# Kernel optimization log

Measured on AMD Instinct MI355X. Metric: run time of the kernel, lower is better.

Reference implementation:

```python
import jax, jax.numpy as jnp
import numpy as np

B, T, C, H, N = 4, 1024, 2048, 32, 64
DFF, DW, DV, DA, DG = 8192, 64, 32, 64, 128
GN_EPS = 64e-5  # RWKV7 ln_x GroupNorm eps


def _ln(x, w, b, eps=1e-5):
    m = x.mean(-1, keepdims=True)
    v = ((x - m) ** 2).mean(-1, keepdims=True)
    return (x - m) / jnp.sqrt(v + eps) * w + b


def _block(x, v_first, att_shift, ffn_shift, wkv_state,
           ln1_w, ln1_b, ln2_w, ln2_b,
           x_r, x_w, x_k, x_v, x_a, x_g,
           Wr, Wk, Wv, Wo,
           w0, w1, w2, v0, v1, v2, a0, a1, a2, g1, g2,
           k_k, k_a, r_k, lnx_w, lnx_b,
           ffn_xk, Wk_ffn, Wv_ffn):
    # ----- TimeMix -----
    xn = _ln(x, ln1_w, ln1_b)
    xx = jnp.concatenate([att_shift[:, None, :], xn[:, :-1]], axis=1) - xn
    xr = xn + xx * x_r
    xw = xn + xx * x_w
    xk_ = xn + xx * x_k
    xv = xn + xx * x_v
    xa = xn + xx * x_a
    xg = xn + xx * x_g

    r = xr @ Wr
    w = -jax.nn.softplus(-(w0 + jnp.tanh(xw @ w1) @ w2)) - 0.5  # <= -0.5
    k = xk_ @ Wk
    v = xv @ Wv
    # layer_id != 0: interpolate toward v_first
    v = v + (v_first - v) * jax.nn.sigmoid(v0 + (xv @ v1) @ v2)
    a = jax.nn.sigmoid(a0 + (xa @ a1) @ a2)
    g = jax.nn.sigmoid(xg @ g1) @ g2

    kk = (k * k_k).reshape(B, T, H, N)
    kk = kk / jnp.maximum(jnp.linalg.norm(kk, axis=-1, keepdims=True), 1e-12)
    k = k * (1.0 + (a - 1.0) * k_a)

    rh = r.reshape(B, T, H, N)
    wh = jnp.exp(-jnp.exp(w.reshape(B, T, H, N)))  # decay in (0,1)
    kh = k.reshape(B, T, H, N)
    vh = v.reshape(B, T, H, N)
    ah = a.reshape(B, T, H, N)
    aa = -kk
    bb = kk * ah

    def step(S, inp):
        # S: [B,H,N(value),N(key)]
        r_t, w_t, k_t, v_t, a_t, b_t = inp
        sa = jnp.einsum('bhvk,bhk->bhv', S, a_t)
        S = S * w_t[:, :, None, :] + sa[..., None] * b_t[:, :, None, :] + v_t[..., None] * k_t[:, :, None, :]
        y = jnp.einsum('bhvk,bhk->bhv', S, r_t)
        return S, y

    tm = lambda z: jnp.swapaxes(z, 0, 1)  # [B,T,H,N] -> [T,B,H,N]
    S_new, ys = jax.lax.scan(step, wkv_state, (tm(rh), tm(wh), tm(kh), tm(vh), tm(aa), tm(bb)))
    x_wkv = jnp.swapaxes(ys, 0, 1).reshape(B, T, C)

    # GroupNorm over H groups of size N (RWKV7 ln_x)
    xh = x_wkv.reshape(B, T, H, N)
    mu = xh.mean(-1, keepdims=True)
    var = ((xh - mu) ** 2).mean(-1, keepdims=True)
    x_wkv = ((xh - mu) / jnp.sqrt(var + GN_EPS)).reshape(B, T, C) * lnx_w + lnx_b

    resid = ((rh * kh * r_k).sum(-1, keepdims=True) * vh).reshape(B, T, C)
    x_wkv = x_wkv + resid
    att_out = (x_wkv * g) @ Wo
    x1 = x + att_out

    # ----- ChannelMix -----
    xn2 = _ln(x1, ln2_w, ln2_b)
    xx2 = jnp.concatenate([ffn_shift[:, None, :], xn2[:, :-1]], axis=1) - xn2
    xkf = xn2 + xx2 * ffn_xk
    kf = jnp.square(jax.nn.relu(xkf @ Wk_ffn))
    x_out = x1 + kf @ Wv_ffn
    return x_out, S_new


def setup_inputs() -> dict:
    ks = jax.random.split(jax.random.key(0), 48)
    rn = lambda i, sh, s=1.0: jax.random.normal(ks[i], sh, dtype=jnp.float32) * s
    return {
        'x': rn(0, (B, T, C)), 'v_first': rn(1, (B, T, C)),
        'att_shift': rn(2, (B, C)), 'ffn_shift': rn(3, (B, C)),
        'wkv_state': jnp.zeros((B, H, N, N), jnp.float32),
        'ln1_w': jnp.ones((C,), jnp.float32), 'ln1_b': jnp.zeros((C,), jnp.float32),
        'ln2_w': jnp.ones((C,), jnp.float32), 'ln2_b': jnp.zeros((C,), jnp.float32),
        'x_r': rn(4, (C,), 0.3), 'x_w': rn(5, (C,), 0.3), 'x_k': rn(6, (C,), 0.3),
        'x_v': rn(7, (C,), 0.3), 'x_a': rn(8, (C,), 0.3), 'x_g': rn(9, (C,), 0.3),
        'Wr': rn(10, (C, C), 0.02), 'Wk': rn(11, (C, C), 0.02),
        'Wv': rn(12, (C, C), 0.02), 'Wo': rn(13, (C, C), 0.02),
        'w0': rn(14, (C,), 0.3), 'w1': rn(15, (C, DW), 0.02), 'w2': rn(16, (DW, C), 0.02),
        'v0': rn(17, (C,), 0.3), 'v1': rn(18, (C, DV), 0.02), 'v2': rn(19, (DV, C), 0.02),
        'a0': rn(20, (C,), 0.3), 'a1': rn(21, (C, DA), 0.02), 'a2': rn(22, (DA, C), 0.02),
        'g1': rn(23, (C, DG), 0.02), 'g2': rn(24, (DG, C), 0.02),
        'k_k': rn(25, (C,), 0.1) + 0.7, 'k_a': rn(26, (C,), 0.1) + 0.7, 'r_k': rn(27, (H, N), 0.1),
        'lnx_w': jnp.ones((C,), jnp.float32), 'lnx_b': jnp.zeros((C,), jnp.float32),
        'ffn_xk': rn(28, (C,), 0.3), 'Wk_ffn': rn(29, (C, DFF), 0.02), 'Wv_ffn': rn(30, (DFF, C), 0.02),
    }


def reference(x, v_first, att_shift, ffn_shift, wkv_state,
              ln1_w, ln1_b, ln2_w, ln2_b,
              x_r, x_w, x_k, x_v, x_a, x_g,
              Wr, Wk, Wv, Wo,
              w0, w1, w2, v0, v1, v2, a0, a1, a2, g1, g2,
              k_k, k_a, r_k, lnx_w, lnx_b,
              ffn_xk, Wk_ffn, Wv_ffn):
    return _block(x, v_first, att_shift, ffn_shift, wkv_state,
                  ln1_w, ln1_b, ln2_w, ln2_b,
                  x_r, x_w, x_k, x_v, x_a, x_g,
                  Wr, Wk, Wv, Wo,
                  w0, w1, w2, v0, v1, v2, a0, a1, a2, g1, g2,
                  k_k, k_a, r_k, lnx_w, lnx_b,
                  ffn_xk, Wk_ffn, Wv_ffn)
```

## Files before the change

### kernel.cpp

```cpp
#include <hip/hip_runtime.h>
#include <cstdint>


typedef __attribute__((ext_vector_type(4))) float f32x4;
typedef __attribute__((ext_vector_type(8))) __bf16 bf16x8;
typedef __attribute__((ext_vector_type(8))) unsigned short us8;

#define DEV __device__ __forceinline__

DEV unsigned short f2b(float f) {
  union { float f; unsigned u; } v; v.f = f;
  unsigned r = v.u + 0x7fffu + ((v.u >> 16) & 1u);
  return (unsigned short)(r >> 16);
}
DEV float b2f(unsigned short u) {
  union { unsigned u; float f; } v; v.u = (unsigned)u << 16;
  return v.f;
}

DEV void gload16(const void* g, void* l) {
  void* gg = const_cast<void*>(g);
  __builtin_amdgcn_global_load_lds(
      (__attribute__((address_space(1))) unsigned int*)gg,
      (__attribute__((address_space(3))) unsigned int*)l, 16, 0, 0);
}

DEV float red8(float v) {
  v += __shfl_xor(v, 1);
  v += __shfl_xor(v, 2);
  v += __shfl_xor(v, 4);
  return v;
}


__global__ void k_transpose(const float* __restrict__ src,
                            unsigned short* __restrict__ dst, int R, int Cc) {
  __shared__ float tile[32][33];
  const int c0 = blockIdx.x * 32, r0 = blockIdx.y * 32;
  const int tx = threadIdx.x, ty = threadIdx.y;
  for (int i = ty; i < 32; i += 8)
    tile[i][tx] = src[(size_t)(r0 + i) * Cc + c0 + tx];
  __syncthreads();
  for (int i = ty; i < 32; i += 8)
    dst[(size_t)(c0 + i) * R + r0 + tx] = f2b(tile[tx][i]);
}

__global__ void k_wcat(const float* __restrict__ w1, const float* __restrict__ a1,
                       const float* __restrict__ v1, const float* __restrict__ g1,
                       const float* __restrict__ xw, const float* __restrict__ xa,
                       const float* __restrict__ xv, const float* __restrict__ xg,
                       unsigned short* __restrict__ dst) {
  const int i = blockIdx.x * 256 + threadIdx.x;
  if (i >= 384 * 4096) return;
  const int j = i >> 12, c = i & 4095;
  float val = 0.f;
  if (j < 288) {
    const float* W; const float* mix; int jj, D;
    if (j < 64)       { W = w1; mix = xw; jj = j;       D = 64;  }
    else if (j < 128) { W = a1; mix = xa; jj = j - 64;  D = 64;  }
    else if (j < 160) { W = v1; mix = xv; jj = j - 128; D = 32;  }
    else              { W = g1; mix = xg; jj = j - 160; D = 128; }
    const int cc = c & 2047;
    val = W[(size_t)cc * D + jj];
    if (c >= 2048) val *= mix[cc];
  }
  dst[i] = f2b(val);
}


DEV void breduce2(float& a, float& b, float* rbuf) {
#pragma unroll
  for (int m = 1; m < 64; m <<= 1) { a += __shfl_xor(a, m); b += __shfl_xor(b, m); }
  const int wid = threadIdx.x >> 6, lane = threadIdx.x & 63;
  if (lane == 0) { rbuf[wid] = a; rbuf[4 + wid] = b; }
  __syncthreads();
  a = rbuf[0] + rbuf[1] + rbuf[2] + rbuf[3];
  b = rbuf[4] + rbuf[5] + rbuf[6] + rbuf[7];
  __syncthreads();
}

__global__ __launch_bounds__(256)
void k_ln1_mix(const float* __restrict__ x, const float* __restrict__ shift,
               const float* __restrict__ lw, const float* __restrict__ lb,
               const float* __restrict__ mr, const float* __restrict__ mk,
               const float* __restrict__ mv,
               unsigned short* __restrict__ A2, unsigned short* __restrict__ xrb,
               unsigned short* __restrict__ xkb, unsigned short* __restrict__ xvb) {
  __shared__ float rbuf[8];
  const int m = blockIdx.x, tid = threadIdx.x;
  const int b = m >> 10, t = m & 1023;
  const float* xt = x + (size_t)m * 2048 + tid * 8;
  const float* xp = (t > 0) ? (x + (size_t)(m - 1) * 2048 + tid * 8)
                            : (shift + (size_t)b * 2048 + tid * 8);
  float vt[8], vp[8];
  *(float4*)&vt[0] = *(const float4*)(xt);
  *(float4*)&vt[4] = *(const float4*)(xt + 4);
  *(float4*)&vp[0] = *(const float4*)(xp);
  *(float4*)&vp[4] = *(const float4*)(xp + 4);
  float st = 0.f, sp = 0.f;
#pragma unroll
  for (int i = 0; i < 8; ++i) { st += vt[i]; sp += vp[i]; }
  breduce2(st, sp, rbuf);
  const float mt_ = st * (1.f / 2048.f), mp_ = sp * (1.f / 2048.f);
  float qt = 0.f, qp = 0.f;
#pragma unroll
  for (int i = 0; i < 8; ++i) {
    float d0 = vt[i] - mt_; qt += d0 * d0;
    float d1 = vp[i] - mp_; qp += d1 * d1;
  }
  breduce2(qt, qp, rbuf);
  const float rt = rsqrtf(qt * (1.f / 2048.f) + 1e-5f);
  const float rp = rsqrtf(qp * (1.f / 2048.f) + 1e-5f);
  const bool lnp = (t > 0);
#pragma unroll
  for (int i = 0; i < 8; ++i) {
    const int c = tid * 8 + i;
    const float wv = lw[c], bv = lb[c];
    const float xn = (vt[i] - mt_) * rt * wv + bv;
    const float pn = lnp ? ((vp[i] - mp_) * rp * wv + bv) : vp[i];
    const float xx = pn - xn;
    A2[(size_t)m * 4096 + c] = f2b(xn);
    A2[(size_t)m * 4096 + 2048 + c] = f2b(xx);
    xrb[(size_t)m * 2048 + c] = f2b(xn + xx * mr[c]);
    xkb[(size_t)m * 2048 + c] = f2b(xn + xx * mk[c]);
    xvb[(size_t)m * 2048 + c] = f2b(xn + xx * mv[c]);
  }
}

__global__ __launch_bounds__(256)
void k_ln2_mix(const float* __restrict__ x1, const float* __restrict__ shift,
               const float* __restrict__ lw, const float* __restrict__ lb,
               const float* __restrict__ mk, unsigned short* __restrict__ xkf) {
  __shared__ float rbuf[8];
  const int m = blockIdx.x, tid = threadIdx.x;
  const int b = m >> 10, t = m & 1023;
  const float* xt = x1 + (size_t)m * 2048 + tid * 8;
  const float* xp = (t > 0) ? (x1 + (size_t)(m - 1) * 2048 + tid * 8)
                            : (shift + (size_t)b * 2048 + tid * 8);
  float vt[8], vp[8];
  *(float4*)&vt[0] = *(const float4*)(xt);
  *(float4*)&vt[4] = *(const float4*)(xt + 4);
  *(float4*)&vp[0] = *(const float4*)(xp);
  *(float4*)&vp[4] = *(const float4*)(xp + 4);
  float st = 0.f, sp = 0.f;
#pragma unroll
  for (int i = 0; i < 8; ++i) { st += vt[i]; sp += vp[i]; }
  breduce2(st, sp, rbuf);
  const float mt_ = st * (1.f / 2048.f), mp_ = sp * (1.f / 2048.f);
  float qt = 0.f, qp = 0.f;
#pragma unroll
  for (int i = 0; i < 8; ++i) {
    float d0 = vt[i] - mt_; qt += d0 * d0;
    float d1 = vp[i] - mp_; qp += d1 * d1;
  }
  breduce2(qt, qp, rbuf);
  const float rt = rsqrtf(qt * (1.f / 2048.f) + 1e-5f);
  const float rp = rsqrtf(qp * (1.f / 2048.f) + 1e-5f);
  const bool lnp = (t > 0);
#pragma unroll
  for (int i = 0; i < 8; ++i) {
    const int c = tid * 8 + i;
    const float wv = lw[c], bv = lb[c];
    const float xn = (vt[i] - mt_) * rt * wv + bv;
    const float pn = lnp ? ((vp[i] - mp_) * rp * wv + bv) : vp[i];
    xkf[(size_t)m * 2048 + c] = f2b(xn + (pn - xn) * mk[c]);
  }
}


constexpr int EP_F32 = 0, EP_B16 = 1, EP_W = 2, EP_AB16 = 3, EP_VGB16 = 4,
              EP_RELU2 = 5, EP_ADDF = 6, EP_HACT = 7;

template <int EP>
DEV void ep_store(float acc, long row, long c, long ldc, float* Co,
                  unsigned short* Cob, const float* bias, const float* e0f,
                  const unsigned short* e0b) {
  const long idx = row * ldc + c;
  if constexpr (EP == EP_F32) {
    Co[idx] = acc;
  } else if constexpr (EP == EP_B16) {
    Cob[idx] = f2b(acc);
  } else if constexpr (EP == EP_W) {
    const float wv = bias[c] + acc;
    const float sp = log1pf(expf(-wv));
    const float w = -sp - 0.5f;
    Co[idx] = expf(-expf(w));
  } else if constexpr (EP == EP_AB16) {
    Cob[idx] = f2b(1.f / (1.f + expf(-(bias[c] + acc))));
  } else if constexpr (EP == EP_VGB16) {
    const float s = 1.f / (1.f + expf(-(bias[c] + acc)));
    const float vv = b2f(e0b[idx]);
    Cob[idx] = f2b(vv + (e0f[idx] - vv) * s);
  } else if constexpr (EP == EP_RELU2) {
    const float r = fmaxf(acc, 0.f);
    Cob[idx] = f2b(r * r);
  } else if constexpr (EP == EP_ADDF) {
    Co[idx] = acc + e0f[idx];
  } else if constexpr (EP == EP_HACT) {
    float vv = acc;
    if (c < 64) vv = tanhf(vv);
    else if (c >= 160) vv = 1.f / (1.f + expf(-vv));
    Cob[idx] = f2b(vv);
  }
}

template <int EP>
__global__ __launch_bounds__(256)
void gemm_bt(const unsigned short* __restrict__ A, long lda,
             const unsigned short* __restrict__ Bt, long ldb, long N, long K,
             long ldc, float* __restrict__ Co, unsigned short* __restrict__ Cob,
             const float* __restrict__ bias, const float* __restrict__ e0f,
             const unsigned short* __restrict__ e0b) {
  __shared__ unsigned short As[4096];
  __shared__ unsigned short Bs[4096];
  const int tid = threadIdx.x;
  const int wid = tid >> 6, lane = tid & 63;
  const long row0 = (long)blockIdx.x * 128, col0 = (long)blockIdx.y * 128;
  const int wm = (wid >> 1) * 64, wn = (wid & 1) * 64;
  f32x4 acc[4][4] = {};
  const int sr = tid >> 2, sk = (tid & 3) * 8;
  const unsigned short* gA = A + (row0 + sr) * lda + sk;
  const unsigned short* gB = Bt + (col0 + sr) * ldb + sk;
  unsigned short* lA = As + wid * 512;
  unsigned short* lB = Bs + wid * 512;
  const int fr = lane & 15, fk = (lane >> 4) * 8;

  for (long kb = 0; kb < K; kb += 32) {
    gload16(gA + kb, lA);
    gload16(gA + kb + 64 * lda, lA + 2048);
    gload16(gB + kb, lB);
    gload16(gB + kb + 64 * ldb, lB + 2048);
    __syncthreads();
    bf16x8 af[4], bq[4];
#pragma unroll
    for (int mt = 0; mt < 4; ++mt)
      af[mt] = *(const bf16x8*)(As + (wm + mt * 16 + fr) * 32 + fk);
#pragma unroll
    for (int nt = 0; nt < 4; ++nt)
      bq[nt] = *(const bf16x8*)(Bs + (wn + nt * 16 + fr) * 32 + fk);
#pragma unroll
    for (int mt = 0; mt < 4; ++mt)
#pragma unroll
      for (int nt = 0; nt < 4; ++nt)
        acc[mt][nt] = __builtin_amdgcn_mfma_f32_16x16x32_bf16(
            af[mt], bq[nt], acc[mt][nt], 0, 0, 0);
    __syncthreads();
  }
  const int fq = lane >> 4;
#pragma unroll
  for (int mt = 0; mt < 4; ++mt) {
#pragma unroll
    for (int nt = 0; nt < 4; ++nt) {
      const long c = col0 + wn + nt * 16 + fr;
      if (c < N) {
        const long rb = row0 + wm + mt * 16 + fq * 4;
#pragma unroll
        for (int rg = 0; rg < 4; ++rg)
          ep_store<EP>(acc[mt][nt][rg], rb + rg, c, ldc, Co, Cob, bias, e0f, e0b);
      }
    }
  }
}

__global__ __launch_bounds__(256)
void k_post(unsigned short* __restrict__ kio, unsigned short* __restrict__ abio,
            unsigned short* __restrict__ aao, const float* __restrict__ kkw,
            const float* __restrict__ kaw) {
  const int m = blockIdx.x, tid = threadIdx.x;
  const size_t base = (size_t)m * 2048 + tid * 8;
  us8 k8 = *(const us8*)(kio + base);
  us8 a8 = *(const us8*)(abio + base);
  float kk8[8], ka8[8];
  *(float4*)&kk8[0] = *(const float4*)(kkw + tid * 8);
  *(float4*)&kk8[4] = *(const float4*)(kkw + tid * 8 + 4);
  *(float4*)&ka8[0] = *(const float4*)(kaw + tid * 8);
  *(float4*)&ka8[4] = *(const float4*)(kaw + tid * 8 + 4);
  float kx[8], kv[8], av[8];
  float ss = 0.f;
#pragma unroll
  for (int i = 0; i < 8; ++i) {
    kv[i] = b2f(k8[i]); av[i] = b2f(a8[i]);
    kx[i] = kv[i] * kk8[i]; ss += kx[i] * kx[i];
  }
  ss = red8(ss);
  const float inv = 1.f / fmaxf(sqrtf(ss), 1e-12f);
  us8 kh8, aa8, bb8;
#pragma unroll
  for (int i = 0; i < 8; ++i) {
    const float kkn = kx[i] * inv;
    kh8[i] = f2b(kv[i] * (1.f + (av[i] - 1.f) * ka8[i]));
    aa8[i] = f2b(-kkn);
    bb8[i] = f2b(kkn * av[i]);
  }
  *(us8*)(kio + base) = kh8;
  *(us8*)(aao + base) = aa8;
  *(us8*)(abio + base) = bb8;
}


DEV float red16(float x) {
  union { float f; int i; } a, r;
  a.f = x; r.i = __builtin_amdgcn_update_dpp(0, a.i, 0xB1, 0xf, 0xf, true);
  x += r.f;
  a.f = x; r.i = __builtin_amdgcn_update_dpp(0, a.i, 0x4E, 0xf, 0xf, true);
  x += r.f;
  a.f = x; r.i = __builtin_amdgcn_update_dpp(0, a.i, 0x124, 0xf, 0xf, true);
  x += r.f;
  a.f = x; r.i = __builtin_amdgcn_update_dpp(0, a.i, 0x128, 0xf, 0xf, true);
  x += r.f;
  return x;
}

DEV void cv4(const uint2 q, float* o) {
  union { unsigned u; float f; } t;
  t.u = q.x << 16;          o[0] = t.f;
  t.u = q.x & 0xffff0000u;  o[1] = t.f;
  t.u = q.y << 16;          o[2] = t.f;
  t.u = q.y & 0xffff0000u;  o[3] = t.f;
}

__global__ __launch_bounds__(64)
void k_scan(const unsigned short* __restrict__ rp,
            const unsigned short* __restrict__ kp,
            const unsigned short* __restrict__ vp,
            const float* __restrict__ wp,
            const unsigned short* __restrict__ ap,
            const unsigned short* __restrict__ bp,
            const float* __restrict__ s0, unsigned short* __restrict__ yout,
            float* __restrict__ snew) {
  __shared__ float4 slots[8][49];
  __shared__ unsigned short ylds[1024][4];
  const int lane = threadIdx.x;
  const int bh = blockIdx.x & 127;
  const int rq = blockIdx.x >> 7;
  const int b = bh >> 5, h = bh & 31;
  const int kg = lane & 15, rl = lane >> 4;
  const int v = rq * 4 + rl, ks = kg * 4;
  const size_t off_bh = (size_t)b * 1024 * 2048 + (size_t)h * 64;

  float S[4];
  *(float4*)&S[0] = *(const float4*)(s0 + (((size_t)bh * 64 + v) * 64 + ks));

  const char* gp = nullptr;
  size_t gstep = 0;
  if (lane < 49) {
    if (lane < 32) {
      const int arr = lane >> 3, sub = lane & 7;
      const unsigned short* base = arr == 0 ? rp : arr == 1 ? kp
                                 : arr == 2 ? ap : bp;
      gp = (const char*)(base + off_bh + sub * 8);
      gstep = 4096;
    } else if (lane < 48) {
      gp = (const char*)(wp + off_bh + (lane - 32) * 4);
      gstep = 8192;
    } else {
      gp = (const char*)(vp + off_bh + (rq & ~1) * 4);
      gstep = 4096;
    }
  }
#pragma unroll
  for (int s = 0; s < 8; ++s) {
    if (lane < 49) gload16(gp, &slots[s][0]);
    gp += gstep;
  }

  for (int t = 0; t < 1024; ++t) {
    asm volatile("s_waitcnt vmcnt(7)" ::: "memory");
    const int sl = t & 7;
    const char* sb = (const char*)&slots[sl][0];
    uint2 r2 = *(const uint2*)(sb + kg * 8);
    uint2 k2 = *(const uint2*)(sb + 128 + kg * 8);
    uint2 a2 = *(const uint2*)(sb + 256 + kg * 8);
    uint2 b2 = *(const uint2*)(sb + 384 + kg * 8);
    float4 wf = *(const float4*)(sb + 512 + kg * 16);
    const unsigned short vfu =
        *(const unsigned short*)(sb + 768 + ((rq & 1) * 4 + rl) * 2);
    asm volatile("s_waitcnt lgkmcnt(0)" ::: "memory");
    if (lane < 49) gload16(gp, &slots[sl][0]);
    if (t < 1015) gp += gstep;

    float rr[4], kk[4], av[4], bv[4];
    cv4(r2, rr); cv4(k2, kk); cv4(a2, av); cv4(b2, bv);
    const float vv = b2f(vfu);
    float sa = S[0] * av[0] + S[1] * av[1] + S[2] * av[2] + S[3] * av[3];
    sa = red16(sa);
    float y;
    S[0] = S[0] * wf.x + sa * bv[0] + vv * kk[0]; y  = S[0] * rr[0];
    S[1] = S[1] * wf.y + sa * bv[1] + vv * kk[1]; y += S[1] * rr[1];
    S[2] = S[2] * wf.z + sa * bv[2] + vv * kk[2]; y += S[2] * rr[2];
    S[3] = S[3] * wf.w + sa * bv[3] + vv * kk[3]; y += S[3] * rr[3];
    y = red16(y);
    if (kg == 0) ylds[t][rl] = f2b(y);
  }

  *(float4*)(snew + (((size_t)bh * 64 + v) * 64 + ks)) = *(const float4*)&S[0];
  asm volatile("s_waitcnt lgkmcnt(0)" ::: "memory");
#pragma unroll 4
  for (int it = 0; it < 16; ++it) {
    const int t = lane + it * 64;
    const uint2 val = *(const uint2*)&ylds[t][0];
    *(uint2*)(yout + off_bh + (size_t)t * 2048 + rq * 4) = val;
  }
}


__global__ __launch_bounds__(256)
void k_gn(const unsigned short* __restrict__ y, const unsigned short* __restrict__ r,
          const unsigned short* __restrict__ kh, const unsigned short* __restrict__ vf,
          const unsigned short* __restrict__ g, const float* __restrict__ rk,
          const float* __restrict__ lw, const float* __restrict__ lb,
          unsigned short* __restrict__ ywg) {
  const int m = blockIdx.x, tid = threadIdx.x;
  const size_t base = (size_t)m * 2048 + tid * 8;
  us8 y8 = *(const us8*)(y + base);
  us8 r8 = *(const us8*)(r + base);
  us8 k8 = *(const us8*)(kh + base);
  us8 v8 = *(const us8*)(vf + base);
  us8 g8 = *(const us8*)(g + base);
  float yv[8];
  float rkv[8];
  *(float4*)&rkv[0] = *(const float4*)(rk + tid * 8);
  *(float4*)&rkv[4] = *(const float4*)(rk + tid * 8 + 4);
  float sy = 0.f, sd = 0.f;
#pragma unroll
  for (int i = 0; i < 8; ++i) {
    yv[i] = b2f(y8[i]);
    sy += yv[i];
    sd += b2f(r8[i]) * b2f(k8[i]) * rkv[i];
  }
  sy = red8(sy);
  sd = red8(sd);
  const float mu = sy * (1.f / 64.f);
  float sq = 0.f;
#pragma unroll
  for (int i = 0; i < 8; ++i) { const float d = yv[i] - mu; sq += d * d; }
  sq = red8(sq);
  const float rstd = rsqrtf(sq * (1.f / 64.f) + 64e-5f);
  us8 o8;
#pragma unroll
  for (int i = 0; i < 8; ++i) {
    const int c = tid * 8 + i;
    const float gn = (yv[i] - mu) * rstd * lw[c] + lb[c];
    o8[i] = f2b((gn + sd * b2f(v8[i])) * b2f(g8[i]));
  }
  *(us8*)(ywg + base) = o8;
}


extern "C" void kernel_launch(void* const* d_in, const int* in_sizes, int n_in,
                              void* d_out, int out_size, void* d_ws,
                              size_t ws_size, hipStream_t stream) {
  (void)in_sizes; (void)n_in; (void)out_size; (void)ws_size;
  const float* x         = (const float*)d_in[0];
  const float* v_first   = (const float*)d_in[1];
  const float* att_shift = (const float*)d_in[2];
  const float* ffn_shift = (const float*)d_in[3];
  const float* wkv0      = (const float*)d_in[4];
  const float* ln1w = (const float*)d_in[5];
  const float* ln1b = (const float*)d_in[6];
  const float* ln2w = (const float*)d_in[7];
  const float* ln2b = (const float*)d_in[8];
  const float* x_r = (const float*)d_in[9];
  const float* x_w = (const float*)d_in[10];
  const float* x_k = (const float*)d_in[11];
  const float* x_v = (const float*)d_in[12];
  const float* x_a = (const float*)d_in[13];
  const float* x_g = (const float*)d_in[14];
  const float* Wr = (const float*)d_in[15];
  const float* Wk = (const float*)d_in[16];
  const float* Wv = (const float*)d_in[17];
  const float* Wo = (const float*)d_in[18];
  const float* w0 = (const float*)d_in[19];
  const float* w1 = (const float*)d_in[20];
  const float* w2 = (const float*)d_in[21];
  const float* v0 = (const float*)d_in[22];
  const float* v1 = (const float*)d_in[23];
  const float* v2 = (const float*)d_in[24];
  const float* a0 = (const float*)d_in[25];
  const float* a1 = (const float*)d_in[26];
  const float* a2 = (const float*)d_in[27];
  const float* g1 = (const float*)d_in[28];
  const float* g2 = (const float*)d_in[29];
  const float* k_k = (const float*)d_in[30];
  const float* k_a = (const float*)d_in[31];
  const float* r_k = (const float*)d_in[32];
  const float* lnxw = (const float*)d_in[33];
  const float* lnxb = (const float*)d_in[34];
  const float* ffn_xk = (const float*)d_in[35];
  const float* Wkf = (const float*)d_in[36];
  const float* Wvf = (const float*)d_in[37];

  char* ws = (char*)d_ws;
  constexpr size_t OFF_TWR   = 0;
  constexpr size_t OFF_TWK   = 8388608;
  constexpr size_t OFF_TWV   = 16777216;
  constexpr size_t OFF_TWO   = 25165824;
  constexpr size_t OFF_TW2   = 33554432;
  constexpr size_t OFF_TA2   = 33816576;
  constexpr size_t OFF_TV2   = 34078720;
  constexpr size_t OFF_TG2   = 34209792;
  constexpr size_t OFF_TWCAT = 34734080;
  constexpr size_t OFF_HACT  = 37879808;
  constexpr size_t OFF_GBUF  = 40239104;
  constexpr size_t OFF_WH    = 57016320;
  constexpr size_t OFF_R     = 90570752;
  constexpr size_t OFF_KH    = 107347968;
  constexpr size_t OFF_VF    = 124125184;
  constexpr size_t OFF_AA    = 140902400;
  constexpr size_t OFF_BB    = 157679616;

  unsigned short* tWr = (unsigned short*)(ws + OFF_TWR);
  unsigned short* tWk = (unsigned short*)(ws + OFF_TWK);
  unsigned short* tWv = (unsigned short*)(ws + OFF_TWV);
  unsigned short* tWo = (unsigned short*)(ws + OFF_TWO);
  unsigned short* tw2 = (unsigned short*)(ws + OFF_TW2);
  unsigned short* ta2 = (unsigned short*)(ws + OFF_TA2);
  unsigned short* tv2 = (unsigned short*)(ws + OFF_TV2);
  unsigned short* tg2 = (unsigned short*)(ws + OFF_TG2);
  unsigned short* tWcat = (unsigned short*)(ws + OFF_TWCAT);
  unsigned short* Hact  = (unsigned short*)(ws + OFF_HACT);
  unsigned short* gbuf  = (unsigned short*)(ws + OFF_GBUF);
  unsigned short* tWvfh = (unsigned short*)(ws + OFF_GBUF);
  unsigned short* act2  = (unsigned short*)(ws + OFF_WH);
  float*          whb   = (float*)(ws + OFF_WH);
  unsigned short* ywg   = (unsigned short*)(ws + OFF_WH);
  unsigned short* kf    = (unsigned short*)(ws + OFF_WH);
  unsigned short* bxr   = (unsigned short*)(ws + OFF_AA);
  unsigned short* bxk   = (unsigned short*)(ws + OFF_BB);
  unsigned short* bxv   = (unsigned short*)(ws + OFF_VF);
  unsigned short* rbuf  = (unsigned short*)(ws + OFF_R);
  unsigned short* khb   = (unsigned short*)(ws + OFF_KH);
  unsigned short* vfb   = (unsigned short*)(ws + OFF_VF);
  unsigned short* aab   = (unsigned short*)(ws + OFF_AA);
  unsigned short* bbb   = (unsigned short*)(ws + OFF_BB);
  unsigned short* vraw  = (unsigned short*)(ws + OFF_AA);
  unsigned short* abuf  = (unsigned short*)(ws + OFF_BB);
  float*          x1    = (float*)(ws + OFF_R);
  unsigned short* xkf   = (unsigned short*)(ws + OFF_VF);
  unsigned short* tWkf  = (unsigned short*)(ws + OFF_AA);
  float* out = (float*)d_out;
  float* snew = out + 8388608;

  const dim3 tb(32, 8);
  k_transpose<<<dim3(64, 64), tb, 0, stream>>>(Wr, tWr, 2048, 2048);
  k_transpose<<<dim3(64, 64), tb, 0, stream>>>(Wk, tWk, 2048, 2048);
  k_transpose<<<dim3(64, 64), tb, 0, stream>>>(Wv, tWv, 2048, 2048);
  k_transpose<<<dim3(64, 64), tb, 0, stream>>>(Wo, tWo, 2048, 2048);
  k_transpose<<<dim3(64, 2), tb, 0, stream>>>(w2, tw2, 64, 2048);
  k_transpose<<<dim3(64, 2), tb, 0, stream>>>(a2, ta2, 64, 2048);
  k_transpose<<<dim3(64, 1), tb, 0, stream>>>(v2, tv2, 32, 2048);
  k_transpose<<<dim3(64, 4), tb, 0, stream>>>(g2, tg2, 128, 2048);
  k_wcat<<<6144, 256, 0, stream>>>(w1, a1, v1, g1, x_w, x_a, x_v, x_g, tWcat);

  k_ln1_mix<<<4096, 256, 0, stream>>>(x, att_shift, ln1w, ln1b, x_r, x_k, x_v,
                                      act2, bxr, bxk, bxv);
  gemm_bt<EP_B16><<<dim3(32, 16), 256, 0, stream>>>(
      bxr, 2048, tWr, 2048, 2048, 2048, 2048, nullptr, rbuf, nullptr, nullptr, nullptr);
  gemm_bt<EP_B16><<<dim3(32, 16), 256, 0, stream>>>(
      bxk, 2048, tWk, 2048, 2048, 2048, 2048, nullptr, khb, nullptr, nullptr, nullptr);
  gemm_bt<EP_B16><<<dim3(32, 16), 256, 0, stream>>>(
      bxv, 2048, tWv, 2048, 2048, 2048, 2048, nullptr, vraw, nullptr, nullptr, nullptr);
  gemm_bt<EP_HACT><<<dim3(32, 3), 256, 0, stream>>>(
      act2, 4096, tWcat, 4096, 288, 4096, 288, nullptr, Hact, nullptr, nullptr, nullptr);
  gemm_bt<EP_W><<<dim3(32, 16), 256, 0, stream>>>(
      Hact + 0, 288, tw2, 64, 2048, 64, 2048, whb, nullptr, w0, nullptr, nullptr);
  gemm_bt<EP_AB16><<<dim3(32, 16), 256, 0, stream>>>(
      Hact + 64, 288, ta2, 64, 2048, 64, 2048, nullptr, abuf, a0, nullptr, nullptr);
  gemm_bt<EP_VGB16><<<dim3(32, 16), 256, 0, stream>>>(
      Hact + 128, 288, tv2, 32, 2048, 32, 2048, nullptr, vfb, v0, v_first, vraw);
  gemm_bt<EP_B16><<<dim3(32, 16), 256, 0, stream>>>(
      Hact + 160, 288, tg2, 128, 2048, 128, 2048, nullptr, gbuf, nullptr, nullptr, nullptr);
  k_post<<<4096, 256, 0, stream>>>(khb, abuf, aab, k_k, k_a);

  k_scan<<<2048, 64, 0, stream>>>(rbuf, khb, vfb, whb, aab, bbb, wkv0,
                                  (unsigned short*)out, snew);
  k_gn<<<4096, 256, 0, stream>>>((const unsigned short*)out, rbuf, khb, vfb,
                                 gbuf, r_k, lnxw, lnxb, ywg);

  gemm_bt<EP_ADDF><<<dim3(32, 16), 256, 0, stream>>>(
      ywg, 2048, tWo, 2048, 2048, 2048, 2048, x1, nullptr, nullptr, x, nullptr);

  k_ln2_mix<<<4096, 256, 0, stream>>>(x1, ffn_shift, ln2w, ln2b, ffn_xk, xkf);
  k_transpose<<<dim3(256, 64), tb, 0, stream>>>(Wkf, tWkf, 2048, 8192);
  gemm_bt<EP_RELU2><<<dim3(32, 32), 256, 0, stream>>>(
      xkf, 2048, tWkf, 2048, 4096, 2048, 4096, nullptr, kf, nullptr, nullptr, nullptr);
  k_transpose<<<dim3(64, 128), tb, 0, stream>>>(Wvf, tWvfh, 4096, 2048);
  gemm_bt<EP_ADDF><<<dim3(32, 16), 256, 0, stream>>>(
      kf, 4096, tWvfh, 4096, 2048, 4096, 2048, out, nullptr, nullptr, x1, nullptr);
  gemm_bt<EP_RELU2><<<dim3(32, 32), 256, 0, stream>>>(
      xkf, 2048, tWkf + (size_t)4096 * 2048, 2048, 4096, 2048, 4096, nullptr, kf,
      nullptr, nullptr, nullptr);
  k_transpose<<<dim3(64, 128), tb, 0, stream>>>(Wvf + (size_t)4096 * 2048, tWvfh,
                                                4096, 2048);
  gemm_bt<EP_ADDF><<<dim3(32, 16), 256, 0, stream>>>(
      kf, 4096, tWvfh, 4096, 2048, 4096, 2048, out, nullptr, nullptr, out, nullptr);
}
```

Baseline: 1.355 ms.

## Add double-buffered 128x256 GEMM kernel with swizzled LDS for large projections

Adds a new gemm2 kernel that uses 512 threads and 128x256 output tiles. It double-buffers LDS so the next K-slice's global_load_lds overlaps the current MFMA work, XOR-swizzles LDS columns to cut bank conflicts, and raises wave priority around the MFMA block. The big square projections (r/k/v, output, and both FFN halves) now use this kernel instead of the single-buffered 128x128 gemm_bt. The trade-off is more LDS use per block and fewer blocks, which lowers occupancy and leaves fewer tiles to fill all CUs.

```diff
diff --git a/kernel.cpp b/kernel.cpp
--- a/kernel.cpp
+++ b/kernel.cpp
@@ -204,6 +204,7 @@
   }
 }
 
+
 template <int EP>
 __global__ __launch_bounds__(256)
 void gemm_bt(const unsigned short* __restrict__ A, long lda,
@@ -258,6 +259,85 @@
         for (int rg = 0; rg < 4; ++rg)
           ep_store<EP>(acc[mt][nt][rg], rb + rg, c, ldc, Co, Cob, bias, e0f, e0b);
       }
+    }
+  }
+}
+
+
+template <int EP>
+__global__ __launch_bounds__(512)
+void gemm2(const unsigned short* __restrict__ A, long lda,
+           const unsigned short* __restrict__ Bt, long ldb, long K, long ldc,
+           float* __restrict__ Co, unsigned short* __restrict__ Cob,
+           const float* __restrict__ e0f) {
+  __shared__ unsigned short As[2][4096];
+  __shared__ unsigned short Bs[2][8192];
+  const int tid = threadIdx.x;
+  const int wid = tid >> 6, lane = tid & 63;
+  const long row0 = (long)blockIdx.x * 128, col0 = (long)blockIdx.y * 256;
+  const int wm = (wid >> 2) * 64, wn = (wid & 3) * 64;
+  f32x4 acc[4][4] = {};
+  const int srow = tid >> 2;
+  const int scol = 8 * ((tid & 3) ^ (srow & 3));
+  const unsigned short* gA = A + (row0 + srow) * lda + scol;
+  const unsigned short* gB1 = Bt + (col0 + srow) * ldb + scol;
+  const unsigned short* gB2 = gB1 + 128 * ldb;
+  const int fr = lane & 15, fc = lane >> 4;
+
+#define STAGE2(buf, kb)                                   \
+  {                                                       \
+    gload16(gA + (kb), &As[buf][0] + wid * 512);          \
+    gload16(gB1 + (kb), &Bs[buf][0] + wid * 512);         \
+    gload16(gB2 + (kb), &Bs[buf][0] + 4096 + wid * 512);  \
+  }
+
+  STAGE2(0, 0)
+  const int NT = (int)(K >> 5);
+  int cur = 0;
+  for (int kt = 0; kt < NT; ++kt) {
+    if (kt + 1 < NT) {
+      STAGE2(cur ^ 1, (long)(kt + 1) * 32)
+      asm volatile("s_waitcnt vmcnt(3)" ::: "memory");
+    } else {
+      asm volatile("s_waitcnt vmcnt(0)" ::: "memory");
+    }
+    __builtin_amdgcn_s_barrier();
+    asm volatile("" ::: "memory");
+    bf16x8 af[4], bq[4];
+#pragma unroll
+    for (int mt = 0; mt < 4; ++mt) {
+      const int r = wm + mt * 16 + fr;
+      af[mt] = *(const bf16x8*)(&As[cur][0] + r * 32 + ((fc ^ (r & 3)) * 8));
+    }
+#pragma unroll
+    for (int nt = 0; nt < 4; ++nt) {
+      const int r = wn + nt * 16 + fr;
+      bq[nt] = *(const bf16x8*)(&Bs[cur][0] + r * 32 + ((fc ^ (r & 3)) * 8));
+    }
+    __builtin_amdgcn_s_setprio(1);
+#pragma unroll
+    for (int mt = 0; mt < 4; ++mt)
+#pragma unroll
+      for (int nt = 0; nt < 4; ++nt)
+        acc[mt][nt] = __builtin_amdgcn_mfma_f32_16x16x32_bf16(
+            af[mt], bq[nt], acc[mt][nt], 0, 0, 0);
+    __builtin_amdgcn_s_setprio(0);
+    asm volatile("" ::: "memory");
+    __builtin_amdgcn_s_barrier();
+    cur ^= 1;
+  }
+#undef STAGE2
+  const int fq = lane >> 4;
+#pragma unroll
+  for (int mt = 0; mt < 4; ++mt) {
+#pragma unroll
+    for (int nt = 0; nt < 4; ++nt) {
+      const long c = col0 + wn + nt * 16 + fr;
+      const long rb = row0 + wm + mt * 16 + fq * 4;
+#pragma unroll
+      for (int rg = 0; rg < 4; ++rg)
+        ep_store<EP>(acc[mt][nt][rg], rb + rg, c, ldc, Co, Cob, nullptr, e0f,
+                     nullptr);
     }
   }
 }
@@ -554,12 +634,12 @@
 
   k_ln1_mix<<<4096, 256, 0, stream>>>(x, att_shift, ln1w, ln1b, x_r, x_k, x_v,
                                       act2, bxr, bxk, bxv);
-  gemm_bt<EP_B16><<<dim3(32, 16), 256, 0, stream>>>(
-      bxr, 2048, tWr, 2048, 2048, 2048, 2048, nullptr, rbuf, nullptr, nullptr, nullptr);
-  gemm_bt<EP_B16><<<dim3(32, 16), 256, 0, stream>>>(
-      bxk, 2048, tWk, 2048, 2048, 2048, 2048, nullptr, khb, nullptr, nullptr, nullptr);
-  gemm_bt<EP_B16><<<dim3(32, 16), 256, 0, stream>>>(
-      bxv, 2048, tWv, 2048, 2048, 2048, 2048, nullptr, vraw, nullptr, nullptr, nullptr);
+  gemm2<EP_B16><<<dim3(32, 8), 512, 0, stream>>>(
+      bxr, 2048, tWr, 2048, 2048, 2048, nullptr, rbuf, nullptr);
+  gemm2<EP_B16><<<dim3(32, 8), 512, 0, stream>>>(
+      bxk, 2048, tWk, 2048, 2048, 2048, nullptr, khb, nullptr);
+  gemm2<EP_B16><<<dim3(32, 8), 512, 0, stream>>>(
+      bxv, 2048, tWv, 2048, 2048, 2048, nullptr, vraw, nullptr);
   gemm_bt<EP_HACT><<<dim3(32, 3), 256, 0, stream>>>(
       act2, 4096, tWcat, 4096, 288, 4096, 288, nullptr, Hact, nullptr, nullptr, nullptr);
   gemm_bt<EP_W><<<dim3(32, 16), 256, 0, stream>>>(
@@ -577,21 +657,20 @@
   k_gn<<<4096, 256, 0, stream>>>((const unsigned short*)out, rbuf, khb, vfb,
                                  gbuf, r_k, lnxw, lnxb, ywg);
 
-  gemm_bt<EP_ADDF><<<dim3(32, 16), 256, 0, stream>>>(
-      ywg, 2048, tWo, 2048, 2048, 2048, 2048, x1, nullptr, nullptr, x, nullptr);
+  gemm2<EP_ADDF><<<dim3(32, 8), 512, 0, stream>>>(
+      ywg, 2048, tWo, 2048, 2048, 2048, x1, nullptr, x);
 
   k_ln2_mix<<<4096, 256, 0, stream>>>(x1, ffn_shift, ln2w, ln2b, ffn_xk, xkf);
   k_transpose<<<dim3(256, 64), tb, 0, stream>>>(Wkf, tWkf, 2048, 8192);
-  gemm_bt<EP_RELU2><<<dim3(32, 32), 256, 0, stream>>>(
-      xkf, 2048, tWkf, 2048, 4096, 2048, 4096, nullptr, kf, nullptr, nullptr, nullptr);
+  gemm2<EP_RELU2><<<dim3(32, 16), 512, 0, stream>>>(
+      xkf, 2048, tWkf, 2048, 2048, 4096, nullptr, kf, nullptr);
   k_transpose<<<dim3(64, 128), tb, 0, stream>>>(Wvf, tWvfh, 4096, 2048);
-  gemm_bt<EP_ADDF><<<dim3(32, 16), 256, 0, stream>>>(
-      kf, 4096, tWvfh, 4096, 2048, 4096, 2048, out, nullptr, nullptr, x1, nullptr);
-  gemm_bt<EP_RELU2><<<dim3(32, 32), 256, 0, stream>>>(
-      xkf, 2048, tWkf + (size_t)4096 * 2048, 2048, 4096, 2048, 4096, nullptr, kf,
-      nullptr, nullptr, nullptr);
+  gemm2<EP_ADDF><<<dim3(32, 8), 512, 0, stream>>>(
+      kf, 4096, tWvfh, 4096, 4096, 2048, out, nullptr, x1);
+  gemm2<EP_RELU2><<<dim3(32, 16), 512, 0, stream>>>(
+      xkf, 2048, tWkf + (size_t)4096 * 2048, 2048, 2048, 4096, nullptr, kf, nullptr);
   k_transpose<<<dim3(64, 128), tb, 0, stream>>>(Wvf + (size_t)4096 * 2048, tWvfh,
                                                 4096, 2048);
-  gemm_bt<EP_ADDF><<<dim3(32, 16), 256, 0, stream>>>(
-      kf, 4096, tWvfh, 4096, 2048, 4096, 2048, out, nullptr, nullptr, out, nullptr);
-}
+  gemm2<EP_ADDF><<<dim3(32, 8), 512, 0, stream>>>(
+      kf, 4096, tWvfh, 4096, 4096, 2048, out, nullptr, out);
+}
```

New measurement: 1.277 ms. -5.7%, faster.
